# Kernel optimization log

Hardware: AMD Instinct MI355X
Metric: run time of the kernel (lower is better)

The kernel has to match this reference:

```python
import jax, jax.numpy as jnp
import numpy as np

B, N_IN, D_IN = 64, 2304, 8
J, L = 32, 16  # num_capsules, capsule_dim
ROUTING_ITERS = 3
EPS = 1e-7


def setup_inputs() -> dict:
    key = jax.random.key(0)
    k1, k2 = jax.random.split(key)
    x = jax.random.normal(k1, (B, N_IN, D_IN), dtype=jnp.float32)
    W = jax.random.normal(k2, (N_IN, J, D_IN, L), dtype=jnp.float32) * 0.05
    return {"x": x, "W": W}


def squash(s):
    # s: [B, J, L]
    sq_norm = jnp.sum(jnp.square(s), axis=-1, keepdims=True)
    scale = sq_norm / (1.0 + sq_norm) / jnp.sqrt(sq_norm + EPS)
    return scale * s


def reference(x, W):
    # Faithful to the source: einsum 'bni,njkl->bnjl' sums i and k independently.
    predictions = jnp.einsum('bni,njkl->bnjl', x, W)  # [B, N, J, L]
    b = jnp.zeros((x.shape[0], N_IN, J), dtype=predictions.dtype)
    v = None
    for i in range(ROUTING_ITERS):
        c = jax.nn.softmax(b, axis=2)                       # [B, N, J]
        s = jnp.sum(predictions * c[..., None], axis=1)     # [B, J, L]
        v = squash(s)                                       # [B, J, L]
        if i < ROUTING_ITERS - 1:
            agreement = jnp.einsum('bnjl,bjl->bnj', predictions, v)
            b = b + agreement
    return v
```

## Files before the change

### kernel.cpp

```cpp
#include <hip/hip_runtime.h>

#define B_   64
#define N_   2304
#define J_   32
#define L_   16
#define EPS_ 1e-7f
#define BG   2
#define NSPL 16
#define NSL  144
#define NTHR 512
#define NGRID 512
#define NT   18
#define STR  20


__global__ __launch_bounds__(256) void prep_kernel(const float* __restrict__ x,
                                                   const float* __restrict__ W,
                                                   float* __restrict__ Ws,
                                                   float* __restrict__ xs_g) {
    const int o = blockIdx.x * 256 + threadIdx.x;
    const int NW4 = N_ * J_ * L_ / 4;
    if (o < NW4) {
        const int n = o >> 7, r = o & 127;
        const float4* base = (const float4*)W + (size_t)n * 1024 + (r >> 2) * 32 + (r & 3);
        float4 s = make_float4(0.f, 0.f, 0.f, 0.f);
#pragma unroll
        for (int k = 0; k < 8; ++k) {
            float4 t = base[k * 4];
            s.x += t.x; s.y += t.y; s.z += t.z; s.w += t.w;
        }
        ((float4*)Ws)[o] = s;
    } else {
        const int q = o - NW4;
        if (q < B_ * N_) {
            const float4* p4 = (const float4*)(x + (size_t)q * 8);
            float4 a = p4[0], c = p4[1];
            xs_g[q] = a.x + a.y + a.z + a.w + c.x + c.y + c.z + c.w;
        }
    }
}

template<int T>
__global__ __launch_bounds__(NTHR) void iter_kernel(const float* __restrict__ Ws,
                                                    const float* __restrict__ xs_g,
                                                    const float* __restrict__ pA,
                                                    float* __restrict__ s0g,
                                                    float* __restrict__ pout) {
    __shared__ float xs_lds[BG * NSL];
    __shared__ float u_lds[BG * 544];
    __shared__ float sred[256 * STR];

    const int tid = threadIdx.x;
    const int blk = blockIdx.x;
    const int sp  = ((blk & 7) << 1) | ((blk >> 3) & 1);
    const int bg  = blk >> 4;
    const int bb  = bg * BG;
    const int nb  = sp * NSL;

    if (tid < BG * NSL) {
        const int b4f = tid / NSL, nlf = tid - b4f * NSL;
        xs_lds[tid] = xs_g[(size_t)(bb + b4f) * N_ + nb + nlf];
    }

    const int nl8 = tid >> 6;
    const int b4  = (tid >> 5) & 1;
    const int j   = tid & 31;
    const float* wbase = Ws + (size_t)nb * 512 + j * 16;

    const float4* wr0 = (const float4*)(wbase + (size_t)nl8 * 512);
    float4 w0 = wr0[0], w1 = wr0[1], w2 = wr0[2], w3 = wr0[3];

    if constexpr (T == 1) {
        for (int q = tid; q < BG * 512; q += NTHR) {
            const int ob = q >> 9, jl = q & 511;
            const float* pp = pA + ((size_t)(bb + ob) * NSPL) * 512 + jl;
            float s = 0.f;
#pragma unroll
            for (int i = 0; i < NSPL; ++i) s += pp[i * 512];
            if (sp == 0) s0g[(bb + ob) * 512 + jl] = s;
            float sq = s * s;
#pragma unroll
            for (int off = 1; off <= 8; off <<= 1) sq += __shfl_xor(sq, off);
            u_lds[ob * 544 + (jl >> 4) * 17 + (jl & 15)] =
                s * (sq / (1.f + sq) / sqrtf(sq + EPS_));
        }
    } else if constexpr (T == 2) {
        for (int q = tid; q < BG * 512; q += NTHR) {
            const int ob = q >> 9, jl = q & 511;
            float s = s0g[(bb + ob) * 512 + jl];
            float sq = s * s;
#pragma unroll
            for (int off = 1; off <= 8; off <<= 1) sq += __shfl_xor(sq, off);
            float u = s * (sq / (1.f + sq) / sqrtf(sq + EPS_));
            const float* pp = pA + ((size_t)(bb + ob) * NSPL) * 512 + jl;
            float s1 = 0.f;
#pragma unroll
            for (int i = 0; i < NSPL; ++i) s1 += pp[i * 512];
            float sq1 = s1 * s1;
#pragma unroll
            for (int off = 1; off <= 8; off <<= 1) sq1 += __shfl_xor(sq1, off);
            u += s1 * (sq1 / (1.f + sq1) / sqrtf(sq1 + EPS_));
            u_lds[ob * 544 + (jl >> 4) * 17 + (jl & 15)] = u;
        }
    }
    __syncthreads();

    float u4[16];
    if constexpr (T > 0) {
#pragma unroll
        for (int l = 0; l < 16; ++l) u4[l] = u_lds[b4 * 544 + j * 17 + l];
    }

    float acc[16];
#pragma unroll
    for (int l = 0; l < 16; ++l) acc[l] = 0.f;

    const float* xbase = xs_lds + b4 * NSL;

    for (int tile = 0; tile < NT; ++tile) {
        float4 n0, n1, n2, n3;
        if (tile + 1 < NT) {
            const float4* nx = (const float4*)(wbase + (size_t)((tile + 1) * 8 + nl8) * 512);
            n0 = nx[0]; n1 = nx[1]; n2 = nx[2]; n3 = nx[3];
        }
        const float xsv = xbase[tile * 8 + nl8];
        float wgt;
        if constexpr (T == 0) {
            wgt = xsv * (1.f / 32.f);
        } else {
            float lg = w0.x*u4[0]  + w0.y*u4[1]  + w0.z*u4[2]  + w0.w*u4[3]
                     + w1.x*u4[4]  + w1.y*u4[5]  + w1.z*u4[6]  + w1.w*u4[7]
                     + w2.x*u4[8]  + w2.y*u4[9]  + w2.z*u4[10] + w2.w*u4[11]
                     + w3.x*u4[12] + w3.y*u4[13] + w3.z*u4[14] + w3.w*u4[15];
            lg *= xsv;
            float e = __expf(lg);
            float ss = e;
#pragma unroll
            for (int off = 1; off <= 16; off <<= 1) ss += __shfl_xor(ss, off);
            wgt = (e / ss) * xsv;
        }
        acc[0]  += wgt*w0.x; acc[1]  += wgt*w0.y; acc[2]  += wgt*w0.z; acc[3]  += wgt*w0.w;
        acc[4]  += wgt*w1.x; acc[5]  += wgt*w1.y; acc[6]  += wgt*w1.z; acc[7]  += wgt*w1.w;
        acc[8]  += wgt*w2.x; acc[9]  += wgt*w2.y; acc[10] += wgt*w2.z; acc[11] += wgt*w2.w;
        acc[12] += wgt*w3.x; acc[13] += wgt*w3.y; acc[14] += wgt*w3.z; acc[15] += wgt*w3.w;
        if (tile + 1 < NT) { w0 = n0; w1 = n1; w2 = n2; w3 = n3; }
    }

    if (nl8 >= 4) {
        float* sr = sred + (size_t)(tid - 256) * STR;
        ((float4*)sr)[0] = make_float4(acc[0],  acc[1],  acc[2],  acc[3]);
        ((float4*)sr)[1] = make_float4(acc[4],  acc[5],  acc[6],  acc[7]);
        ((float4*)sr)[2] = make_float4(acc[8],  acc[9],  acc[10], acc[11]);
        ((float4*)sr)[3] = make_float4(acc[12], acc[13], acc[14], acc[15]);
    }
    __syncthreads();
    if (nl8 < 4) {
        float* sr = sred + (size_t)tid * STR;
#pragma unroll
        for (int d = 0; d < 4; ++d) {
            float4 t = ((float4*)sr)[d];
            t.x += acc[d*4+0]; t.y += acc[d*4+1]; t.z += acc[d*4+2]; t.w += acc[d*4+3];
            ((float4*)sr)[d] = t;
        }
    }
    __syncthreads();

    for (int q = tid; q < BG * 512; q += NTHR) {
        const int ob = q >> 9, jl = q & 511;
        const int oj = jl >> 4, ol = jl & 15;
        float s = 0.f;
#pragma unroll
        for (int nl = 0; nl < 4; ++nl)
            s += sred[(size_t)(nl * 64 + ob * 32 + oj) * STR + ol];
        pout[((size_t)(bb + ob) * NSPL + sp) * 512 + jl] = s;
    }
}

__global__ __launch_bounds__(512) void final_kernel(const float* __restrict__ p2,
                                                    float* __restrict__ out) {
    const int g = blockIdx.x * 512 + threadIdx.x;
    const int b = g >> 9, jl = g & 511;
    const float* pp = p2 + ((size_t)b * NSPL) * 512 + jl;
    float s = 0.f;
#pragma unroll
    for (int s2 = 0; s2 < NSPL; ++s2) s += pp[s2 * 512];
    float sq = s * s;
#pragma unroll
    for (int off = 1; off <= 8; off <<= 1) sq += __shfl_xor(sq, off);
    out[g] = s * (sq / (1.f + sq) / sqrtf(sq + EPS_));
}

extern "C" void kernel_launch(void* const* d_in, const int* in_sizes, int n_in,
                              void* d_out, int out_size, void* d_ws, size_t ws_size,
                              hipStream_t stream) {
    const float* x = (const float*)d_in[0];
    const float* W = (const float*)d_in[1];
    float* out = (float*)d_out;

    float* Ws  = (float*)d_ws;
    float* xsg = Ws  + (size_t)N_ * J_ * L_;
    float* p0  = xsg + (size_t)B_ * N_;
    float* p1  = p0  + (size_t)B_ * NSPL * 512;
    float* p2  = p1  + (size_t)B_ * NSPL * 512;
    float* s0  = p2  + (size_t)B_ * NSPL * 512;

    prep_kernel<<<1728, 256, 0, stream>>>(x, W, Ws, xsg);
    iter_kernel<0><<<NGRID, NTHR, 0, stream>>>(Ws, xsg, nullptr, nullptr, p0);
    iter_kernel<1><<<NGRID, NTHR, 0, stream>>>(Ws, xsg, p0, s0, p1);
    iter_kernel<2><<<NGRID, NTHR, 0, stream>>>(Ws, xsg, p1, s0, p2);
    final_kernel<<<64, 512, 0, stream>>>(p2, out);
}
```

Baseline: 75.23 us.

## Process one batch per block and deepen W register prefetch to two tiles

Each iter_kernel block now handles a single batch element with 256 threads instead of two with 512, which doubles the grid to 1024 blocks. The W-row register prefetch now looks two tiles ahead (w/v/n rotation) rather than one, so more global load latency is hidden. The cost is that each W tile is read from global memory once per batch element rather than once per pair, doubling W traffic through L2, and each thread holds more registers for the extra prefetch stage.

After: 86.73 us. 15.3% more time.

```diff
diff --git a/kernel.cpp b/kernel.cpp
--- a/kernel.cpp
+++ b/kernel.cpp
@@ -5,11 +5,10 @@
 #define J_   32
 #define L_   16
 #define EPS_ 1e-7f
-#define BG   2
 #define NSPL 16
 #define NSL  144
-#define NTHR 512
-#define NGRID 512
+#define NTHR 256
+#define NGRID 1024
 #define NT   18
 #define STR  20
 
@@ -46,53 +45,51 @@
                                                     const float* __restrict__ pA,
                                                     float* __restrict__ s0g,
                                                     float* __restrict__ pout) {
-    __shared__ float xs_lds[BG * NSL];
-    __shared__ float u_lds[BG * 544];
-    __shared__ float sred[256 * STR];
+    __shared__ float xs_lds[NSL];
+    __shared__ float u_lds[544];
+    __shared__ float sred[128 * STR];
 
     const int tid = threadIdx.x;
     const int blk = blockIdx.x;
     const int sp  = ((blk & 7) << 1) | ((blk >> 3) & 1);
-    const int bg  = blk >> 4;
-    const int bb  = bg * BG;
+    const int b   = blk >> 4;
     const int nb  = sp * NSL;
 
-    if (tid < BG * NSL) {
-        const int b4f = tid / NSL, nlf = tid - b4f * NSL;
-        xs_lds[tid] = xs_g[(size_t)(bb + b4f) * N_ + nb + nlf];
-    }
-
-    const int nl8 = tid >> 6;
-    const int b4  = (tid >> 5) & 1;
+    if (tid < NSL) xs_lds[tid] = xs_g[(size_t)b * N_ + nb + tid];
+
+    const int nl8 = tid >> 5;
     const int j   = tid & 31;
     const float* wbase = Ws + (size_t)nb * 512 + j * 16;
 
-    const float4* wr0 = (const float4*)(wbase + (size_t)nl8 * 512);
-    float4 w0 = wr0[0], w1 = wr0[1], w2 = wr0[2], w3 = wr0[3];
+    float4 w0, w1, w2, w3, v0, v1, v2, v3;
+    {
+        const float4* t0 = (const float4*)(wbase + (size_t)nl8 * 512);
+        w0 = t0[0]; w1 = t0[1]; w2 = t0[2]; w3 = t0[3];
+        const float4* t1 = (const float4*)(wbase + (size_t)(8 + nl8) * 512);
+        v0 = t1[0]; v1 = t1[1]; v2 = t1[2]; v3 = t1[3];
+    }
 
     if constexpr (T == 1) {
-        for (int q = tid; q < BG * 512; q += NTHR) {
-            const int ob = q >> 9, jl = q & 511;
-            const float* pp = pA + ((size_t)(bb + ob) * NSPL) * 512 + jl;
+        for (int q = tid; q < 512; q += NTHR) {
+            const float* pp = pA + ((size_t)b * NSPL) * 512 + q;
             float s = 0.f;
 #pragma unroll
             for (int i = 0; i < NSPL; ++i) s += pp[i * 512];
-            if (sp == 0) s0g[(bb + ob) * 512 + jl] = s;
+            if (sp == 0) s0g[b * 512 + q] = s;
             float sq = s * s;
 #pragma unroll
             for (int off = 1; off <= 8; off <<= 1) sq += __shfl_xor(sq, off);
-            u_lds[ob * 544 + (jl >> 4) * 17 + (jl & 15)] =
+            u_lds[(q >> 4) * 17 + (q & 15)] =
                 s * (sq / (1.f + sq) / sqrtf(sq + EPS_));
         }
     } else if constexpr (T == 2) {
-        for (int q = tid; q < BG * 512; q += NTHR) {
-            const int ob = q >> 9, jl = q & 511;
-            float s = s0g[(bb + ob) * 512 + jl];
+        for (int q = tid; q < 512; q += NTHR) {
+            float s = s0g[b * 512 + q];
             float sq = s * s;
 #pragma unroll
             for (int off = 1; off <= 8; off <<= 1) sq += __shfl_xor(sq, off);
             float u = s * (sq / (1.f + sq) / sqrtf(sq + EPS_));
-            const float* pp = pA + ((size_t)(bb + ob) * NSPL) * 512 + jl;
+            const float* pp = pA + ((size_t)b * NSPL) * 512 + q;
             float s1 = 0.f;
 #pragma unroll
             for (int i = 0; i < NSPL; ++i) s1 += pp[i * 512];
@@ -100,7 +97,7 @@
 #pragma unroll
             for (int off = 1; off <= 8; off <<= 1) sq1 += __shfl_xor(sq1, off);
             u += s1 * (sq1 / (1.f + sq1) / sqrtf(sq1 + EPS_));
-            u_lds[ob * 544 + (jl >> 4) * 17 + (jl & 15)] = u;
+            u_lds[(q >> 4) * 17 + (q & 15)] = u;
         }
     }
     __syncthreads();
@@ -108,22 +105,20 @@
     float u4[16];
     if constexpr (T > 0) {
 #pragma unroll
-        for (int l = 0; l < 16; ++l) u4[l] = u_lds[b4 * 544 + j * 17 + l];
+        for (int l = 0; l < 16; ++l) u4[l] = u_lds[j * 17 + l];
     }
 
     float acc[16];
 #pragma unroll
     for (int l = 0; l < 16; ++l) acc[l] = 0.f;
 
-    const float* xbase = xs_lds + b4 * NSL;
-
     for (int tile = 0; tile < NT; ++tile) {
-        float4 n0, n1, n2, n3;
-        if (tile + 1 < NT) {
-            const float4* nx = (const float4*)(wbase + (size_t)((tile + 1) * 8 + nl8) * 512);
+        float4 n0 = make_float4(0.f, 0.f, 0.f, 0.f), n1 = n0, n2 = n0, n3 = n0;
+        if (tile + 2 < NT) {
+            const float4* nx = (const float4*)(wbase + (size_t)((tile + 2) * 8 + nl8) * 512);
             n0 = nx[0]; n1 = nx[1]; n2 = nx[2]; n3 = nx[3];
         }
-        const float xsv = xbase[tile * 8 + nl8];
+        const float xsv = xs_lds[tile * 8 + nl8];
         float wgt;
         if constexpr (T == 0) {
             wgt = xsv * (1.f / 32.f);
@@ -143,11 +138,14 @@
         acc[4]  += wgt*w1.x; acc[5]  += wgt*w1.y; acc[6]  += wgt*w1.z; acc[7]  += wgt*w1.w;
         acc[8]  += wgt*w2.x; acc[9]  += wgt*w2.y; acc[10] += wgt*w2.z; acc[11] += wgt*w2.w;
         acc[12] += wgt*w3.x; acc[13] += wgt*w3.y; acc[14] += wgt*w3.z; acc[15] += wgt*w3.w;
-        if (tile + 1 < NT) { w0 = n0; w1 = n1; w2 = n2; w3 = n3; }
+        if (tile + 1 < NT) {
+            w0 = v0; w1 = v1; w2 = v2; w3 = v3;
+            v0 = n0; v1 = n1; v2 = n2; v3 = n3;
+        }
     }
 
     if (nl8 >= 4) {
-        float* sr = sred + (size_t)(tid - 256) * STR;
+        float* sr = sred + (size_t)(tid - 128) * STR;
         ((float4*)sr)[0] = make_float4(acc[0],  acc[1],  acc[2],  acc[3]);
         ((float4*)sr)[1] = make_float4(acc[4],  acc[5],  acc[6],  acc[7]);
         ((float4*)sr)[2] = make_float4(acc[8],  acc[9],  acc[10], acc[11]);
@@ -165,14 +163,13 @@
     }
     __syncthreads();
 
-    for (int q = tid; q < BG * 512; q += NTHR) {
-        const int ob = q >> 9, jl = q & 511;
-        const int oj = jl >> 4, ol = jl & 15;
+    for (int q = tid; q < 512; q += NTHR) {
+        const int oj = q >> 4, ol = q & 15;
         float s = 0.f;
 #pragma unroll
         for (int nl = 0; nl < 4; ++nl)
-            s += sred[(size_t)(nl * 64 + ob * 32 + oj) * STR + ol];
-        pout[((size_t)(bb + ob) * NSPL + sp) * 512 + jl] = s;
+            s += sred[(size_t)(nl * 32 + oj) * STR + ol];
+        pout[((size_t)b * NSPL + sp) * 512 + q] = s;
     }
 }
 
```
